# Kernel tuning notes

Measured on AMD Instinct MI355X. Metric: run time of the kernel, lower is better.

The kernel has to match this reference:

```python
import jax, jax.numpy as jnp
import numpy as np

B, N, D = 16, 2048, 128
SCALE = 1.0 / np.sqrt(D).astype(np.float32)


def setup_inputs() -> dict:
    key = jax.random.key(0)
    ks = jax.random.split(key, 9)
    Q = jax.random.normal(ks[0], (B, N, D), dtype=jnp.float32)
    K = jax.random.normal(ks[1], (B, N, D), dtype=jnp.float32)
    V = jax.random.normal(ks[2], (B, N, D), dtype=jnp.float32)
    bias_dis = 0.1 * jax.random.normal(ks[3], (N, N), dtype=jnp.float32)
    bias_dtw = 0.1 * jax.random.normal(ks[4], (N, N), dtype=jnp.float32)
    bias_pattern = 0.1 * jax.random.normal(ks[5], (N, N), dtype=jnp.float32)
    bias_poi = 0.1 * jax.random.normal(ks[6], (N, N), dtype=jnp.float32)
    # key/query padding masks: mostly True (valid) with some padding
    input_mask = jax.random.randint(ks[7], (B, N), 0, 10) > 0
    embeddings_mask = jax.random.randint(ks[8], (B, N), 0, 10) > 0
    # lower-triangular causal mask (diagonal kept so every row has a valid key)
    causal_mask = jnp.tril(jnp.ones((N, N), dtype=bool))
    return {"Q": Q, "K": K, "V": V, "bias_dis": bias_dis, "bias_dtw": bias_dtw,
            "bias_pattern": bias_pattern, "bias_poi": bias_poi,
            "input_mask": input_mask, "embeddings_mask": embeddings_mask,
            "causal_mask": causal_mask}


def reference(Q, K, V, bias_dis, bias_dtw, bias_pattern, bias_poi,
              input_mask, embeddings_mask, causal_mask):
    # masked_fill_(~mask, 0.0) on K, V with input_mask[:, :, None]
    km = input_mask[:, :, None]
    K = jnp.where(km, K, 0.0)
    V = jnp.where(km, V, 0.0)
    # masked_fill_(~mask, 0.0) on Q with embeddings_mask[:, :, None]
    Q = jnp.where(embeddings_mask[:, :, None], Q, 0.0)
    # scores [B, N, N] = Q K^T / sqrt(dim)
    scores = jnp.einsum('bnd,bmd->bnm', Q, K) * SCALE
    # causal masked_fill_(~causal_mask, -inf)
    scores = jnp.where(causal_mask[None, :, :], scores, -jnp.inf)
    # per-batch bias loop == broadcast add of summed [N, N] biases
    scores = scores + (bias_dis + bias_dtw + bias_pattern + bias_poi)[None, :, :]
    P = jax.nn.softmax(scores, axis=-1)
    # dropout p=0 (eval) -> identity
    return jnp.einsum('bnm,bmd->bnd', P, V)
```

## Files before the change

### kernel.cpp

```cpp
#include <hip/hip_runtime.h>
#include <math.h>

constexpr int Bc = 16;
constexpr int Nc = 2048;
constexpr int Dc = 128;
constexpr int NCHUNK = Nc / 64;
constexpr float SCALE_F = 0.08838834764831845f;

typedef __bf16 bf16x8 __attribute__((ext_vector_type(8)));
typedef __bf16 bf16x4 __attribute__((ext_vector_type(4)));
typedef float  f32x4  __attribute__((ext_vector_type(4)));

constexpr size_t KPACK_BYTES = (size_t)Bc * NCHUNK * 16 * 64 * 16;
constexpr size_t VPACK_BYTES = KPACK_BYTES;
constexpr size_t BIAS_BYTES  = (size_t)Nc * Nc * 4;
constexpr int CHUNK_ELEMS = 16 * 64 * 8;

__device__ __forceinline__ void gload_lds16(const __bf16* gsrc, __bf16* ldst) {
    __builtin_amdgcn_global_load_lds(
        (const __attribute__((address_space(1))) unsigned int*)gsrc,
        (__attribute__((address_space(3))) unsigned int*)ldst, 16, 0, 0);
}

__global__ __launch_bounds__(256) void bias_sum_kernel(
    const float* __restrict__ b0, const float* __restrict__ b1,
    const float* __restrict__ b2, const float* __restrict__ b3,
    float* __restrict__ bs)
{
    const int i = blockIdx.x * 256 + threadIdx.x;
    const float4 a = ((const float4*)b0)[i];
    const float4 c = ((const float4*)b1)[i];
    const float4 d = ((const float4*)b2)[i];
    const float4 e = ((const float4*)b3)[i];
    float4 r;
    r.x = a.x + c.x + d.x + e.x;
    r.y = a.y + c.y + d.y + e.y;
    r.z = a.z + c.z + d.z + e.z;
    r.w = a.w + c.w + d.w + e.w;
    ((float4*)bs)[i] = r;
}

__global__ __launch_bounds__(256) void pack_kv(
    const float* __restrict__ K, const float* __restrict__ V,
    const int* __restrict__ imask,
    __bf16* __restrict__ Kp, __bf16* __restrict__ Vp)
{
    __shared__ __align__(16) __bf16 Ks[64][136];
    __shared__ __align__(16) __bf16 Vs[64][136];
    const int tid = threadIdx.x;
    const int c = blockIdx.x, b = blockIdx.y;
    const int m0 = c * 64;
    const float* Kb = K + (size_t)b * Nc * Dc;
    const float* Vb = V + (size_t)b * Nc * Dc;
    const int* imb = imask + b * Nc;

    #pragma unroll
    for (int it = 0; it < 8; ++it) {
        const int idx = it * 256 + tid;
        const int row = idx >> 5;
        const int c4  = idx & 31;
        const int gm  = m0 + row;
        const float msk = imb[gm] ? 1.0f : 0.0f;
        const float4 kf = ((const float4*)(Kb + (size_t)gm * Dc))[c4];
        const float4 vf = ((const float4*)(Vb + (size_t)gm * Dc))[c4];
        bf16x4 kb, vb;
        kb[0] = (__bf16)(kf.x * msk); kb[1] = (__bf16)(kf.y * msk);
        kb[2] = (__bf16)(kf.z * msk); kb[3] = (__bf16)(kf.w * msk);
        vb[0] = (__bf16)(vf.x * msk); vb[1] = (__bf16)(vf.y * msk);
        vb[2] = (__bf16)(vf.z * msk); vb[3] = (__bf16)(vf.w * msk);
        *(bf16x4*)&Ks[row][c4 * 4] = kb;
        *(bf16x4*)&Vs[row][c4 * 4] = vb;
    }
    __syncthreads();

    const size_t chunk_base = (size_t)(b * NCHUNK + c) * CHUNK_ELEMS;
    #pragma unroll
    for (int i = 0; i < 4; ++i) {
        const int s = i * 256 + tid;
        const int f = s >> 6;
        const int l = s & 63;
        const int quad = (l >> 4) & 3;
        const int l15  = l & 15;
        {
            const int jt = f >> 2, kd = f & 3;
            const bf16x8 kv = *(const bf16x8*)&Ks[jt * 16 + l15][kd * 32 + quad * 8];
            *(bf16x8*)&Kp[chunk_base + (size_t)f * 512 + l * 8] = kv;
        }
        {
            const int kj = f >> 3, dt = f & 7;
            bf16x8 vv;
            #pragma unroll
            for (int j = 0; j < 8; ++j)
                vv[j] = Vs[kj * 32 + quad * 8 + j][dt * 16 + l15];
            *(bf16x8*)&Vp[chunk_base + (size_t)f * 512 + l * 8] = vv;
        }
    }
}

__global__ __launch_bounds__(256) void attn_packed(
    const float* __restrict__ Q,
    const __bf16* __restrict__ Kp, const __bf16* __restrict__ Vp,
    const float* __restrict__ p0, const float* __restrict__ p1,
    const float* __restrict__ p2, const float* __restrict__ p3,
    const int* __restrict__ emask, float* __restrict__ out, int nbias)
{
    __shared__ __align__(16) __bf16 Kl[16 * 512];
    __shared__ __align__(16) __bf16 Vl[16 * 512];
    __shared__ __align__(16) __bf16 Pl[4][16][72];

    const int tid  = threadIdx.x;
    const int w    = tid >> 6;
    const int lane = tid & 63;
    const int quad = lane >> 4;
    const int l15  = lane & 15;
    const int x = blockIdx.x, y = blockIdx.y;
    const int ti = (y < 8) ? x : (31 - x);
    const int b  = ((y & 7) << 1) | (y >> 3);
    const int q0  = ti * 64;
    const int q0w = q0 + w * 16;

    const float* Qb = Q + (size_t)b * Nc * Dc;

    bf16x8 qfrag[4];
    {
        const int row = q0w + l15;
        const float qs = emask[b * Nc + row] ? SCALE_F : 0.0f;
        const float4* qr = (const float4*)(Qb + (size_t)row * Dc);
        #pragma unroll
        for (int kd = 0; kd < 4; ++kd) {
            const float4 xx = qr[kd * 8 + quad * 2];
            const float4 yy = qr[kd * 8 + quad * 2 + 1];
            qfrag[kd][0] = (__bf16)(xx.x * qs); qfrag[kd][1] = (__bf16)(xx.y * qs);
            qfrag[kd][2] = (__bf16)(xx.z * qs); qfrag[kd][3] = (__bf16)(xx.w * qs);
            qfrag[kd][4] = (__bf16)(yy.x * qs); qfrag[kd][5] = (__bf16)(yy.y * qs);
            qfrag[kd][6] = (__bf16)(yy.z * qs); qfrag[kd][7] = (__bf16)(yy.w * qs);
        }
    }

    f32x4 oacc[8];
    #pragma unroll
    for (int dt = 0; dt < 8; ++dt) { oacc[dt][0]=0.f; oacc[dt][1]=0.f; oacc[dt][2]=0.f; oacc[dt][3]=0.f; }
    float mrun[4] = {-INFINITY, -INFINITY, -INFINITY, -INFINITY};
    float lrun[4] = {0.f, 0.f, 0.f, 0.f};

    for (int c = 0; c <= ti; ++c) {
        const int m0 = c * 64;
        __syncthreads();

        const __bf16* gK = Kp + (size_t)(b * NCHUNK + c) * CHUNK_ELEMS;
        const __bf16* gV = Vp + (size_t)(b * NCHUNK + c) * CHUNK_ELEMS;
        #pragma unroll
        for (int i = 0; i < 4; ++i) {
            const int seg = w * 4 + i;
            gload_lds16(gK + seg * 512 + lane * 8, Kl + seg * 512);
            gload_lds16(gV + seg * 512 + lane * 8, Vl + seg * 512);
        }

        float bsv[4][4];
        #pragma unroll
        for (int jt = 0; jt < 4; ++jt) {
            #pragma unroll
            for (int reg = 0; reg < 4; ++reg) {
                const int gr = q0w + quad * 4 + reg;
                const size_t boff = (size_t)gr * Nc + m0 + jt * 16 + l15;
                float v = p0[boff];
                if (nbias == 4) v += p1[boff] + p2[boff] + p3[boff];
                bsv[jt][reg] = v;
            }
        }
        __syncthreads();

        f32x4 sc[4];
        #pragma unroll
        for (int jt = 0; jt < 4; ++jt) { sc[jt][0]=0.f; sc[jt][1]=0.f; sc[jt][2]=0.f; sc[jt][3]=0.f; }
        #pragma unroll
        for (int jt = 0; jt < 4; ++jt) {
            #pragma unroll
            for (int kd = 0; kd < 4; ++kd) {
                const bf16x8 bfr = *(const bf16x8*)&Kl[(jt * 4 + kd) * 512 + lane * 8];
                sc[jt] = __builtin_amdgcn_mfma_f32_16x16x32_bf16(qfrag[kd], bfr, sc[jt], 0, 0, 0);
            }
        }

        if (c == ti) {
            #pragma unroll
            for (int jt = 0; jt < 4; ++jt)
                #pragma unroll
                for (int reg = 0; reg < 4; ++reg) {
                    const int gr = q0w + quad * 4 + reg;
                    const int gc = m0 + jt * 16 + l15;
                    const float s = sc[jt][reg] + bsv[jt][reg];
                    sc[jt][reg] = (gc > gr) ? -INFINITY : s;
                }
        } else {
            #pragma unroll
            for (int jt = 0; jt < 4; ++jt)
                #pragma unroll
                for (int reg = 0; reg < 4; ++reg)
                    sc[jt][reg] += bsv[jt][reg];
        }

        float mloc[4];
        #pragma unroll
        for (int reg = 0; reg < 4; ++reg)
            mloc[reg] = fmaxf(fmaxf(sc[0][reg], sc[1][reg]), fmaxf(sc[2][reg], sc[3][reg]));
        #pragma unroll
        for (int off = 1; off <= 8; off <<= 1)
            #pragma unroll
            for (int reg = 0; reg < 4; ++reg)
                mloc[reg] = fmaxf(mloc[reg], __shfl_xor(mloc[reg], off, 64));
        float lloc[4];
        #pragma unroll
        for (int reg = 0; reg < 4; ++reg) {
            const float mn = fmaxf(mrun[reg], mloc[reg]);
            const float alpha = __expf(mrun[reg] - mn);
            mrun[reg] = mn;
            lrun[reg] *= alpha;
            #pragma unroll
            for (int dt = 0; dt < 8; ++dt) oacc[dt][reg] *= alpha;
            float ls = 0.f;
            #pragma unroll
            for (int jt = 0; jt < 4; ++jt) {
                const float pv = __expf(sc[jt][reg] - mn);
                sc[jt][reg] = pv;
                ls += pv;
            }
            lloc[reg] = ls;
        }
        #pragma unroll
        for (int off = 1; off <= 8; off <<= 1)
            #pragma unroll
            for (int reg = 0; reg < 4; ++reg)
                lloc[reg] += __shfl_xor(lloc[reg], off, 64);
        #pragma unroll
        for (int reg = 0; reg < 4; ++reg) lrun[reg] += lloc[reg];

        #pragma unroll
        for (int jt = 0; jt < 4; ++jt)
            #pragma unroll
            for (int reg = 0; reg < 4; ++reg)
                Pl[w][quad * 4 + reg][jt * 16 + l15] = (__bf16)sc[jt][reg];

        #pragma unroll
        for (int kj = 0; kj < 2; ++kj) {
            const bf16x8 pa = *(const bf16x8*)&Pl[w][l15][kj * 32 + quad * 8];
            #pragma unroll
            for (int dt = 0; dt < 8; ++dt) {
                const bf16x8 vb = *(const bf16x8*)&Vl[(kj * 8 + dt) * 512 + lane * 8];
                oacc[dt] = __builtin_amdgcn_mfma_f32_16x16x32_bf16(pa, vb, oacc[dt], 0, 0, 0);
            }
        }
    }

    #pragma unroll
    for (int reg = 0; reg < 4; ++reg) {
        const float inv = 1.0f / lrun[reg];
        const int gr = q0w + quad * 4 + reg;
        float* orow = out + ((size_t)b * Nc + gr) * Dc;
        #pragma unroll
        for (int dt = 0; dt < 8; ++dt)
            orow[dt * 16 + l15] = oacc[dt][reg] * inv;
    }
}

__global__ __launch_bounds__(256) void attn_mfma_legacy(
    const float* __restrict__ Q, const float* __restrict__ K, const float* __restrict__ V,
    const float* __restrict__ p0, const float* __restrict__ p1,
    const float* __restrict__ p2, const float* __restrict__ p3,
    const int* __restrict__ imask, const int* __restrict__ emask,
    float* __restrict__ out, int nbias)
{
    __shared__ __align__(16) __bf16 Klds[64][136];
    __shared__ __align__(16) __bf16 Vt[128][72];
    __shared__ __align__(16) __bf16 Plds[4][16][72];
    const int tid  = threadIdx.x;
    const int w    = tid >> 6;
    const int lane = tid & 63;
    const int quad = lane >> 6 ? 0 : (lane >> 4);
    const int l15  = lane & 15;
    const int b = blockIdx.y;
    const int x = blockIdx.x, yy = blockIdx.y;
    const int ti = (yy < 8) ? x : (31 - x);
    const int q0 = ti * 64, q0w = q0 + w * 16;
    const float* Qb = Q + (size_t)b * Nc * Dc;
    const float* Kb = K + (size_t)b * Nc * Dc;
    const float* Vb = V + (size_t)b * Nc * Dc;
    const int* imb = imask + b * Nc;

    bf16x8 qfrag[4];
    {
        const int row = q0w + l15;
        const float qs = emask[b * Nc + row] ? SCALE_F : 0.0f;
        const float4* qr = (const float4*)(Qb + (size_t)row * Dc);
        #pragma unroll
        for (int kd = 0; kd < 4; ++kd) {
            const float4 xv = qr[kd * 8 + quad * 2];
            const float4 yv = qr[kd * 8 + quad * 2 + 1];
            qfrag[kd][0]=(__bf16)(xv.x*qs); qfrag[kd][1]=(__bf16)(xv.y*qs);
            qfrag[kd][2]=(__bf16)(xv.z*qs); qfrag[kd][3]=(__bf16)(xv.w*qs);
            qfrag[kd][4]=(__bf16)(yv.x*qs); qfrag[kd][5]=(__bf16)(yv.y*qs);
            qfrag[kd][6]=(__bf16)(yv.z*qs); qfrag[kd][7]=(__bf16)(yv.w*qs);
        }
    }
    f32x4 oacc[8];
    #pragma unroll
    for (int dt = 0; dt < 8; ++dt){oacc[dt][0]=0.f;oacc[dt][1]=0.f;oacc[dt][2]=0.f;oacc[dt][3]=0.f;}
    float mrun[4]={-INFINITY,-INFINITY,-INFINITY,-INFINITY}, lrun[4]={0.f,0.f,0.f,0.f};

    for (int m0 = 0; m0 <= q0; m0 += 64) {
        __syncthreads();
        #pragma unroll
        for (int it = 0; it < 8; ++it) {
            const int idx = it * 256 + tid;
            const int row = idx >> 5, c4 = idx & 31;
            const int gm = m0 + row;
            const float msk = imb[gm] ? 1.0f : 0.0f;
            const float4 kf = ((const float4*)(Kb + (size_t)gm * Dc))[c4];
            const float4 vf = ((const float4*)(Vb + (size_t)gm * Dc))[c4];
            bf16x4 kb;
            kb[0]=(__bf16)(kf.x*msk); kb[1]=(__bf16)(kf.y*msk);
            kb[2]=(__bf16)(kf.z*msk); kb[3]=(__bf16)(kf.w*msk);
            *(bf16x4*)&Klds[row][c4*4] = kb;
            Vt[c4*4+0][row]=(__bf16)(vf.x*msk); Vt[c4*4+1][row]=(__bf16)(vf.y*msk);
            Vt[c4*4+2][row]=(__bf16)(vf.z*msk); Vt[c4*4+3][row]=(__bf16)(vf.w*msk);
        }
        __syncthreads();
        f32x4 sc[4];
        #pragma unroll
        for (int jt = 0; jt < 4; ++jt){sc[jt][0]=0.f;sc[jt][1]=0.f;sc[jt][2]=0.f;sc[jt][3]=0.f;}
        #pragma unroll
        for (int jt = 0; jt < 4; ++jt)
            #pragma unroll
            for (int kd = 0; kd < 4; ++kd) {
                const bf16x8 bfr = *(const bf16x8*)&Klds[jt*16+l15][kd*32+quad*8];
                sc[jt] = __builtin_amdgcn_mfma_f32_16x16x32_bf16(qfrag[kd], bfr, sc[jt], 0, 0, 0);
            }
        #pragma unroll
        for (int jt = 0; jt < 4; ++jt)
            #pragma unroll
            for (int reg = 0; reg < 4; ++reg) {
                const int gr = q0w + quad*4 + reg;
                const int gc = m0 + jt*16 + l15;
                const size_t boff = (size_t)gr * Nc + gc;
                float bsx = p0[boff];
                if (nbias == 4) bsx += p1[boff] + p2[boff] + p3[boff];
                const float s = sc[jt][reg] + bsx;
                sc[jt][reg] = (gc > gr) ? -INFINITY : s;
            }
        float mloc[4];
        #pragma unroll
        for (int reg = 0; reg < 4; ++reg)
            mloc[reg] = fmaxf(fmaxf(sc[0][reg], sc[1][reg]), fmaxf(sc[2][reg], sc[3][reg]));
        #pragma unroll
        for (int off = 1; off <= 8; off <<= 1)
            #pragma unroll
            for (int reg = 0; reg < 4; ++reg)
                mloc[reg] = fmaxf(mloc[reg], __shfl_xor(mloc[reg], off, 64));
        float lloc[4];
        #pragma unroll
        for (int reg = 0; reg < 4; ++reg) {
            const float mn = fmaxf(mrun[reg], mloc[reg]);
            const float alpha = __expf(mrun[reg] - mn);
            mrun[reg] = mn; lrun[reg] *= alpha;
            #pragma unroll
            for (int dt = 0; dt < 8; ++dt) oacc[dt][reg] *= alpha;
            float ls = 0.f;
            #pragma unroll
            for (int jt = 0; jt < 4; ++jt) {
                const float pv = __expf(sc[jt][reg] - mn);
                sc[jt][reg] = pv; ls += pv;
            }
            lloc[reg] = ls;
        }
        #pragma unroll
        for (int off = 1; off <= 8; off <<= 1)
            #pragma unroll
            for (int reg = 0; reg < 4; ++reg)
                lloc[reg] += __shfl_xor(lloc[reg], off, 64);
        #pragma unroll
        for (int reg = 0; reg < 4; ++reg) lrun[reg] += lloc[reg];
        #pragma unroll
        for (int jt = 0; jt < 4; ++jt)
            #pragma unroll
            for (int reg = 0; reg < 4; ++reg)
                Plds[w][quad*4+reg][jt*16+l15] = (__bf16)sc[jt][reg];
        #pragma unroll
        for (int kj = 0; kj < 2; ++kj) {
            const bf16x8 pa = *(const bf16x8*)&Plds[w][l15][kj*32+quad*8];
            #pragma unroll
            for (int dt = 0; dt < 8; ++dt) {
                const bf16x8 vb = *(const bf16x8*)&Vt[dt*16+l15][kj*32+quad*8];
                oacc[dt] = __builtin_amdgcn_mfma_f32_16x16x32_bf16(pa, vb, oacc[dt], 0, 0, 0);
            }
        }
    }
    #pragma unroll
    for (int reg = 0; reg < 4; ++reg) {
        const float inv = 1.0f / lrun[reg];
        const int gr = q0w + quad*4 + reg;
        float* orow = out + ((size_t)b * Nc + gr) * Dc;
        #pragma unroll
        for (int dt = 0; dt < 8; ++dt)
            orow[dt*16+l15] = oacc[dt][reg] * inv;
    }
}

extern "C" void kernel_launch(void* const* d_in, const int* in_sizes, int n_in,
                              void* d_out, int out_size, void* d_ws, size_t ws_size,
                              hipStream_t stream) {
    const float* Q  = (const float*)d_in[0];
    const float* K  = (const float*)d_in[1];
    const float* V  = (const float*)d_in[2];
    const float* b0 = (const float*)d_in[3];
    const float* b1 = (const float*)d_in[4];
    const float* b2 = (const float*)d_in[5];
    const float* b3 = (const float*)d_in[6];
    const int* im   = (const int*)d_in[7];
    const int* em   = (const int*)d_in[8];
    float* out      = (float*)d_out;

    const dim3 grid(NCHUNK, Bc);
    const bool havePacks = ws_size >= KPACK_BYTES + VPACK_BYTES;
    const bool haveBias  = ws_size >= KPACK_BYTES + VPACK_BYTES + BIAS_BYTES;

    if (havePacks) {
        __bf16* Kp = (__bf16*)d_ws;
        __bf16* Vp = (__bf16*)((char*)d_ws + KPACK_BYTES);
        pack_kv<<<grid, 256, 0, stream>>>(K, V, im, Kp, Vp);
        if (haveBias) {
            float* bs = (float*)((char*)d_ws + KPACK_BYTES + VPACK_BYTES);
            bias_sum_kernel<<<(Nc * Nc / 4) / 256, 256, 0, stream>>>(b0, b1, b2, b3, bs);
            attn_packed<<<grid, 256, 0, stream>>>(Q, Kp, Vp, bs, bs, bs, bs, em, out, 1);
        } else {
            attn_packed<<<grid, 256, 0, stream>>>(Q, Kp, Vp, b0, b1, b2, b3, em, out, 4);
        }
    } else if (ws_size >= BIAS_BYTES) {
        float* bs = (float*)d_ws;
        bias_sum_kernel<<<(Nc * Nc / 4) / 256, 256, 0, stream>>>(b0, b1, b2, b3, bs);
        attn_mfma_legacy<<<grid, 256, 0, stream>>>(Q, K, V, bs, bs, bs, bs, im, em, out, 1);
    } else {
        attn_mfma_legacy<<<grid, 256, 0, stream>>>(Q, K, V, b0, b1, b2, b3, im, em, out, 4);
    }
}
```

Measured before the change: 237.1 us.

## Fuse prep kernels, pair causal query tiles per block, double-buffer K/V loads

Merges the K/V packing and bias-summing kernels into one launch to save a launch and let the two jobs overlap. The attention kernel now gives each block two query tiles (p and 31-p) of the same batch so every block does equal causal work, using a 16x16 grid instead of 32x16. K/V chunks are double-buffered in LDS and the next chunk's bias is prefetched into registers while the current chunk is computed, hiding load latency. The cost is half as many blocks (256), which may lower occupancy and parallelism on a large GPU, plus more LDS and register use.

```diff
diff --git a/kernel.cpp b/kernel.cpp
--- a/kernel.cpp
+++ b/kernel.cpp
@@ -22,33 +22,35 @@
         (__attribute__((address_space(3))) unsigned int*)ldst, 16, 0, 0);
 }
 
-__global__ __launch_bounds__(256) void bias_sum_kernel(
+__global__ __launch_bounds__(256) void prep_fused(
+    const float* __restrict__ K, const float* __restrict__ V,
+    const int* __restrict__ imask,
     const float* __restrict__ b0, const float* __restrict__ b1,
     const float* __restrict__ b2, const float* __restrict__ b3,
-    float* __restrict__ bs)
-{
-    const int i = blockIdx.x * 256 + threadIdx.x;
-    const float4 a = ((const float4*)b0)[i];
-    const float4 c = ((const float4*)b1)[i];
-    const float4 d = ((const float4*)b2)[i];
-    const float4 e = ((const float4*)b3)[i];
-    float4 r;
-    r.x = a.x + c.x + d.x + e.x;
-    r.y = a.y + c.y + d.y + e.y;
-    r.z = a.z + c.z + d.z + e.z;
-    r.w = a.w + c.w + d.w + e.w;
-    ((float4*)bs)[i] = r;
-}
-
-__global__ __launch_bounds__(256) void pack_kv(
-    const float* __restrict__ K, const float* __restrict__ V,
-    const int* __restrict__ imask,
-    __bf16* __restrict__ Kp, __bf16* __restrict__ Vp)
+    __bf16* __restrict__ Kp, __bf16* __restrict__ Vp, float* __restrict__ bs)
 {
     __shared__ __align__(16) __bf16 Ks[64][136];
     __shared__ __align__(16) __bf16 Vs[64][136];
+    const int bid = blockIdx.x;
     const int tid = threadIdx.x;
-    const int c = blockIdx.x, b = blockIdx.y;
+
+    if (bid >= 512) {
+        const int i = (bid - 512) * 256 + tid;
+        const float4 a = ((const float4*)b0)[i];
+        const float4 c = ((const float4*)b1)[i];
+        const float4 d = ((const float4*)b2)[i];
+        const float4 e = ((const float4*)b3)[i];
+        float4 r;
+        r.x = a.x + c.x + d.x + e.x;
+        r.y = a.y + c.y + d.y + e.y;
+        r.z = a.z + c.z + d.z + e.z;
+        r.w = a.w + c.w + d.w + e.w;
+        ((float4*)bs)[i] = r;
+        return;
+    }
+
+    const int c = bid & 31;
+    const int b = bid >> 5;
     const int m0 = c * 64;
     const float* Kb = K + (size_t)b * Nc * Dc;
     const float* Vb = V + (size_t)b * Nc * Dc;
@@ -97,15 +99,14 @@
     }
 }
 
-__global__ __launch_bounds__(256) void attn_packed(
+__global__ __launch_bounds__(256) void attn_paired(
     const float* __restrict__ Q,
     const __bf16* __restrict__ Kp, const __bf16* __restrict__ Vp,
-    const float* __restrict__ p0, const float* __restrict__ p1,
-    const float* __restrict__ p2, const float* __restrict__ p3,
-    const int* __restrict__ emask, float* __restrict__ out, int nbias)
+    const float* __restrict__ bias, const int* __restrict__ emask,
+    float* __restrict__ out)
 {
-    __shared__ __align__(16) __bf16 Kl[16 * 512];
-    __shared__ __align__(16) __bf16 Vl[16 * 512];
+    __shared__ __align__(16) __bf16 Kl[2][16 * 512];
+    __shared__ __align__(16) __bf16 Vl[2][16 * 512];
     __shared__ __align__(16) __bf16 Pl[4][16][72];
 
     const int tid  = threadIdx.x;
@@ -113,153 +114,179 @@
     const int lane = tid & 63;
     const int quad = lane >> 4;
     const int l15  = lane & 15;
-    const int x = blockIdx.x, y = blockIdx.y;
-    const int ti = (y < 8) ? x : (31 - x);
-    const int b  = ((y & 7) << 1) | (y >> 3);
-    const int q0  = ti * 64;
-    const int q0w = q0 + w * 16;
-
-    const float* Qb = Q + (size_t)b * Nc * Dc;
-
-    bf16x8 qfrag[4];
-    {
-        const int row = q0w + l15;
-        const float qs = emask[b * Nc + row] ? SCALE_F : 0.0f;
-        const float4* qr = (const float4*)(Qb + (size_t)row * Dc);
-        #pragma unroll
-        for (int kd = 0; kd < 4; ++kd) {
-            const float4 xx = qr[kd * 8 + quad * 2];
-            const float4 yy = qr[kd * 8 + quad * 2 + 1];
-            qfrag[kd][0] = (__bf16)(xx.x * qs); qfrag[kd][1] = (__bf16)(xx.y * qs);
-            qfrag[kd][2] = (__bf16)(xx.z * qs); qfrag[kd][3] = (__bf16)(xx.w * qs);
-            qfrag[kd][4] = (__bf16)(yy.x * qs); qfrag[kd][5] = (__bf16)(yy.y * qs);
-            qfrag[kd][6] = (__bf16)(yy.z * qs); qfrag[kd][7] = (__bf16)(yy.w * qs);
-        }
-    }
-
-    f32x4 oacc[8];
-    #pragma unroll
-    for (int dt = 0; dt < 8; ++dt) { oacc[dt][0]=0.f; oacc[dt][1]=0.f; oacc[dt][2]=0.f; oacc[dt][3]=0.f; }
-    float mrun[4] = {-INFINITY, -INFINITY, -INFINITY, -INFINITY};
-    float lrun[4] = {0.f, 0.f, 0.f, 0.f};
-
-    for (int c = 0; c <= ti; ++c) {
-        const int m0 = c * 64;
-        __syncthreads();
-
-        const __bf16* gK = Kp + (size_t)(b * NCHUNK + c) * CHUNK_ELEMS;
-        const __bf16* gV = Vp + (size_t)(b * NCHUNK + c) * CHUNK_ELEMS;
+    const int b = blockIdx.x;
+    const int p = blockIdx.y;
+
+    const float*  Qb  = Q + (size_t)b * Nc * Dc;
+    const int*    emb = emask + b * Nc;
+    const __bf16* Kpb = Kp + (size_t)b * NCHUNK * CHUNK_ELEMS;
+    const __bf16* Vpb = Vp + (size_t)b * NCHUNK * CHUNK_ELEMS;
+
+    for (int t = 0; t < 2; ++t) {
+        const int ti  = t ? (31 - p) : p;
+        const int q0w = ti * 64 + w * 16;
+        const int nch = ti + 1;
+
+        bf16x8 qfrag[4];
+        {
+            const int row = q0w + l15;
+            const float qs = emb[row] ? SCALE_F : 0.0f;
+            const float4* qr = (const float4*)(Qb + (size_t)row * Dc);
+            #pragma unroll
+            for (int kd = 0; kd < 4; ++kd) {
+                const float4 xx = qr[kd * 8 + quad * 2];
+                const float4 yy = qr[kd * 8 + quad * 2 + 1];
+                qfrag[kd][0] = (__bf16)(xx.x * qs); qfrag[kd][1] = (__bf16)(xx.y * qs);
+                qfrag[kd][2] = (__bf16)(xx.z * qs); qfrag[kd][3] = (__bf16)(xx.w * qs);
+                qfrag[kd][4] = (__bf16)(yy.x * qs); qfrag[kd][5] = (__bf16)(yy.y * qs);
+                qfrag[kd][6] = (__bf16)(yy.z * qs); qfrag[kd][7] = (__bf16)(yy.w * qs);
+            }
+        }
+
+        f32x4 oacc[8];
+        #pragma unroll
+        for (int dt = 0; dt < 8; ++dt) { oacc[dt][0]=0.f; oacc[dt][1]=0.f; oacc[dt][2]=0.f; oacc[dt][3]=0.f; }
+        float mrun[4] = {-INFINITY, -INFINITY, -INFINITY, -INFINITY};
+        float lrun[4] = {0.f, 0.f, 0.f, 0.f};
+
         #pragma unroll
         for (int i = 0; i < 4; ++i) {
             const int seg = w * 4 + i;
-            gload_lds16(gK + seg * 512 + lane * 8, Kl + seg * 512);
-            gload_lds16(gV + seg * 512 + lane * 8, Vl + seg * 512);
-        }
-
-        float bsv[4][4];
-        #pragma unroll
-        for (int jt = 0; jt < 4; ++jt) {
+            gload_lds16(Kpb + seg * 512 + lane * 8, &Kl[0][seg * 512]);
+            gload_lds16(Vpb + seg * 512 + lane * 8, &Vl[0][seg * 512]);
+        }
+        float bcur[4][4];
+        #pragma unroll
+        for (int jt = 0; jt < 4; ++jt)
+            #pragma unroll
+            for (int reg = 0; reg < 4; ++reg)
+                bcur[jt][reg] = bias[(size_t)(q0w + quad * 4 + reg) * Nc + jt * 16 + l15];
+        __syncthreads();
+
+        for (int c = 0; c < nch; ++c) {
+            const int cb = c & 1;
+            const bool more = (c + 1) < nch;
+
+            if (more) {
+                const size_t off = (size_t)(c + 1) * CHUNK_ELEMS;
+                #pragma unroll
+                for (int i = 0; i < 4; ++i) {
+                    const int seg = w * 4 + i;
+                    gload_lds16(Kpb + off + seg * 512 + lane * 8, &Kl[cb ^ 1][seg * 512]);
+                    gload_lds16(Vpb + off + seg * 512 + lane * 8, &Vl[cb ^ 1][seg * 512]);
+                }
+            }
+            float bnext[4][4];
+            if (more) {
+                const int m1 = (c + 1) * 64;
+                #pragma unroll
+                for (int jt = 0; jt < 4; ++jt)
+                    #pragma unroll
+                    for (int reg = 0; reg < 4; ++reg)
+                        bnext[jt][reg] = bias[(size_t)(q0w + quad * 4 + reg) * Nc + m1 + jt * 16 + l15];
+            }
+
+            f32x4 sc[4];
+            #pragma unroll
+            for (int jt = 0; jt < 4; ++jt) { sc[jt][0]=0.f; sc[jt][1]=0.f; sc[jt][2]=0.f; sc[jt][3]=0.f; }
+            #pragma unroll
+            for (int jt = 0; jt < 4; ++jt)
+                #pragma unroll
+                for (int kd = 0; kd < 4; ++kd) {
+                    const bf16x8 bfr = *(const bf16x8*)&Kl[cb][(jt * 4 + kd) * 512 + lane * 8];
+                    sc[jt] = __builtin_amdgcn_mfma_f32_16x16x32_bf16(qfrag[kd], bfr, sc[jt], 0, 0, 0);
+                }
+
+            if (c == ti) {
+                const int m0 = c * 64;
+                #pragma unroll
+                for (int jt = 0; jt < 4; ++jt)
+                    #pragma unroll
+                    for (int reg = 0; reg < 4; ++reg) {
+                        const int gr = q0w + quad * 4 + reg;
+                        const int gc = m0 + jt * 16 + l15;
+                        const float s = sc[jt][reg] + bcur[jt][reg];
+                        sc[jt][reg] = (gc > gr) ? -INFINITY : s;
+                    }
+            } else {
+                #pragma unroll
+                for (int jt = 0; jt < 4; ++jt)
+                    #pragma unroll
+                    for (int reg = 0; reg < 4; ++reg)
+                        sc[jt][reg] += bcur[jt][reg];
+            }
+
+            float mloc[4];
+            #pragma unroll
+            for (int reg = 0; reg < 4; ++reg)
+                mloc[reg] = fmaxf(fmaxf(sc[0][reg], sc[1][reg]), fmaxf(sc[2][reg], sc[3][reg]));
+            #pragma unroll
+            for (int off = 1; off <= 8; off <<= 1)
+                #pragma unroll
+                for (int reg = 0; reg < 4; ++reg)
+                    mloc[reg] = fmaxf(mloc[reg], __shfl_xor(mloc[reg], off, 64));
+            float lloc[4];
             #pragma unroll
             for (int reg = 0; reg < 4; ++reg) {
-                const int gr = q0w + quad * 4 + reg;
-                const size_t boff = (size_t)gr * Nc + m0 + jt * 16 + l15;
-                float v = p0[boff];
-                if (nbias == 4) v += p1[boff] + p2[boff] + p3[boff];
-                bsv[jt][reg] = v;
-            }
-        }
-        __syncthreads();
-
-        f32x4 sc[4];
-        #pragma unroll
-        for (int jt = 0; jt < 4; ++jt) { sc[jt][0]=0.f; sc[jt][1]=0.f; sc[jt][2]=0.f; sc[jt][3]=0.f; }
-        #pragma unroll
-        for (int jt = 0; jt < 4; ++jt) {
-            #pragma unroll
-            for (int kd = 0; kd < 4; ++kd) {
-                const bf16x8 bfr = *(const bf16x8*)&Kl[(jt * 4 + kd) * 512 + lane * 8];
-                sc[jt] = __builtin_amdgcn_mfma_f32_16x16x32_bf16(qfrag[kd], bfr, sc[jt], 0, 0, 0);
-            }
-        }
-
-        if (c == ti) {
+                const float mn = fmaxf(mrun[reg], mloc[reg]);
+                const float alpha = __expf(mrun[reg] - mn);
+                mrun[reg] = mn;
+                lrun[reg] *= alpha;
+                #pragma unroll
+                for (int dt = 0; dt < 8; ++dt) oacc[dt][reg] *= alpha;
+                float ls = 0.f;
+                #pragma unroll
+                for (int jt = 0; jt < 4; ++jt) {
+                    const float pv = __expf(sc[jt][reg] - mn);
+                    sc[jt][reg] = pv;
+                    ls += pv;
+                }
+                lloc[reg] = ls;
+            }
+            #pragma unroll
+            for (int off = 1; off <= 8; off <<= 1)
+                #pragma unroll
+                for (int reg = 0; reg < 4; ++reg)
+                    lloc[reg] += __shfl_xor(lloc[reg], off, 64);
+            #pragma unroll
+            for (int reg = 0; reg < 4; ++reg) lrun[reg] += lloc[reg];
+
             #pragma unroll
             for (int jt = 0; jt < 4; ++jt)
                 #pragma unroll
-                for (int reg = 0; reg < 4; ++reg) {
-                    const int gr = q0w + quad * 4 + reg;
-                    const int gc = m0 + jt * 16 + l15;
-                    const float s = sc[jt][reg] + bsv[jt][reg];
-                    sc[jt][reg] = (gc > gr) ? -INFINITY : s;
+                for (int reg = 0; reg < 4; ++reg)
+                    Pl[w][quad * 4 + reg][jt * 16 + l15] = (__bf16)sc[jt][reg];
+
+            #pragma unroll
+            for (int kj = 0; kj < 2; ++kj) {
+                const bf16x8 pa = *(const bf16x8*)&Pl[w][l15][kj * 32 + quad * 8];
+                #pragma unroll
+                for (int dt = 0; dt < 8; ++dt) {
+                    const bf16x8 vb = *(const bf16x8*)&Vl[cb][(kj * 8 + dt) * 512 + lane * 8];
+                    oacc[dt] = __builtin_amdgcn_mfma_f32_16x16x32_bf16(pa, vb, oacc[dt], 0, 0, 0);
                 }
-        } else {
-            #pragma unroll
-            for (int jt = 0; jt < 4; ++jt)
-                #pragma unroll
-                for (int reg = 0; reg < 4; ++reg)
-                    sc[jt][reg] += bsv[jt][reg];
-        }
-
-        float mloc[4];
-        #pragma unroll
-        for (int reg = 0; reg < 4; ++reg)
-            mloc[reg] = fmaxf(fmaxf(sc[0][reg], sc[1][reg]), fmaxf(sc[2][reg], sc[3][reg]));
-        #pragma unroll
-        for (int off = 1; off <= 8; off <<= 1)
-            #pragma unroll
-            for (int reg = 0; reg < 4; ++reg)
-                mloc[reg] = fmaxf(mloc[reg], __shfl_xor(mloc[reg], off, 64));
-        float lloc[4];
+            }
+
+            __syncthreads();
+
+            if (more) {
+                #pragma unroll
+                for (int jt = 0; jt < 4; ++jt)
+                    #pragma unroll
+                    for (int reg = 0; reg < 4; ++reg)
+                        bcur[jt][reg] = bnext[jt][reg];
+            }
+        }
+
         #pragma unroll
         for (int reg = 0; reg < 4; ++reg) {
-            const float mn = fmaxf(mrun[reg], mloc[reg]);
-            const float alpha = __expf(mrun[reg] - mn);
-            mrun[reg] = mn;
-            lrun[reg] *= alpha;
-            #pragma unroll
-            for (int dt = 0; dt < 8; ++dt) oacc[dt][reg] *= alpha;
-            float ls = 0.f;
-            #pragma unroll
-            for (int jt = 0; jt < 4; ++jt) {
-                const float pv = __expf(sc[jt][reg] - mn);
-                sc[jt][reg] = pv;
-                ls += pv;
-            }
-            lloc[reg] = ls;
-        }
-        #pragma unroll
-        for (int off = 1; off <= 8; off <<= 1)
-            #pragma unroll
-            for (int reg = 0; reg < 4; ++reg)
-                lloc[reg] += __shfl_xor(lloc[reg], off, 64);
-        #pragma unroll
-        for (int reg = 0; reg < 4; ++reg) lrun[reg] += lloc[reg];
-
-        #pragma unroll
-        for (int jt = 0; jt < 4; ++jt)
-            #pragma unroll
-            for (int reg = 0; reg < 4; ++reg)
-                Pl[w][quad * 4 + reg][jt * 16 + l15] = (__bf16)sc[jt][reg];
-
-        #pragma unroll
-        for (int kj = 0; kj < 2; ++kj) {
-            const bf16x8 pa = *(const bf16x8*)&Pl[w][l15][kj * 32 + quad * 8];
-            #pragma unroll
-            for (int dt = 0; dt < 8; ++dt) {
-                const bf16x8 vb = *(const bf16x8*)&Vl[(kj * 8 + dt) * 512 + lane * 8];
-                oacc[dt] = __builtin_amdgcn_mfma_f32_16x16x32_bf16(pa, vb, oacc[dt], 0, 0, 0);
-            }
-        }
-    }
-
-    #pragma unroll
-    for (int reg = 0; reg < 4; ++reg) {
-        const float inv = 1.0f / lrun[reg];
-        const int gr = q0w + quad * 4 + reg;
-        float* orow = out + ((size_t)b * Nc + gr) * Dc;
-        #pragma unroll
-        for (int dt = 0; dt < 8; ++dt)
-            orow[dt * 16 + l15] = oacc[dt][reg] * inv;
+            const float inv = 1.0f / lrun[reg];
+            const int gr = q0w + quad * 4 + reg;
+            float* orow = out + ((size_t)b * Nc + gr) * Dc;
+            #pragma unroll
+            for (int dt = 0; dt < 8; ++dt)
+                orow[dt * 16 + l15] = oacc[dt][reg] * inv;
+        }
     }
 }
 
@@ -268,7 +295,7 @@
     const float* __restrict__ p0, const float* __restrict__ p1,
     const float* __restrict__ p2, const float* __restrict__ p3,
     const int* __restrict__ imask, const int* __restrict__ emask,
-    float* __restrict__ out, int nbias)
+    float* __restrict__ out)
 {
     __shared__ __align__(16) __bf16 Klds[64][136];
     __shared__ __align__(16) __bf16 Vt[128][72];
@@ -276,7 +303,7 @@
     const int tid  = threadIdx.x;
     const int w    = tid >> 6;
     const int lane = tid & 63;
-    const int quad = lane >> 6 ? 0 : (lane >> 4);
+    const int quad = lane >> 4;
     const int l15  = lane & 15;
     const int b = blockIdx.y;
     const int x = blockIdx.x, yy = blockIdx.y;
@@ -342,8 +369,7 @@
                 const int gr = q0w + quad*4 + reg;
                 const int gc = m0 + jt*16 + l15;
                 const size_t boff = (size_t)gr * Nc + gc;
-                float bsx = p0[boff];
-                if (nbias == 4) bsx += p1[boff] + p2[boff] + p3[boff];
+                const float bsx = p0[boff] + p1[boff] + p2[boff] + p3[boff];
                 const float s = sc[jt][reg] + bsx;
                 sc[jt][reg] = (gc > gr) ? -INFINITY : s;
             }
@@ -419,26 +445,15 @@
     const int* em   = (const int*)d_in[8];
     float* out      = (float*)d_out;
 
-    const dim3 grid(NCHUNK, Bc);
-    const bool havePacks = ws_size >= KPACK_BYTES + VPACK_BYTES;
-    const bool haveBias  = ws_size >= KPACK_BYTES + VPACK_BYTES + BIAS_BYTES;
-
-    if (havePacks) {
+    if (ws_size >= KPACK_BYTES + VPACK_BYTES + BIAS_BYTES) {
         __bf16* Kp = (__bf16*)d_ws;
         __bf16* Vp = (__bf16*)((char*)d_ws + KPACK_BYTES);
-        pack_kv<<<grid, 256, 0, stream>>>(K, V, im, Kp, Vp);
-        if (haveBias) {
-            float* bs = (float*)((char*)d_ws + KPACK_BYTES + VPACK_BYTES);
-            bias_sum_kernel<<<(Nc * Nc / 4) / 256, 256, 0, stream>>>(b0, b1, b2, b3, bs);
-            attn_packed<<<grid, 256, 0, stream>>>(Q, Kp, Vp, bs, bs, bs, bs, em, out, 1);
-        } else {
-            attn_packed<<<grid, 256, 0, stream>>>(Q, Kp, Vp, b0, b1, b2, b3, em, out, 4);
-        }
-    } else if (ws_size >= BIAS_BYTES) {
-        float* bs = (float*)d_ws;
-        bias_sum_kernel<<<(Nc * Nc / 4) / 256, 256, 0, stream>>>(b0, b1, b2, b3, bs);
-        attn_mfma_legacy<<<grid, 256, 0, stream>>>(Q, K, V, bs, bs, bs, bs, im, em, out, 1);
+        float*  bs = (float*)((char*)d_ws + KPACK_BYTES + VPACK_BYTES);
+        prep_fused<<<512 + (Nc * Nc / 4) / 256, 256, 0, stream>>>(
+            K, V, im, b0, b1, b2, b3, Kp, Vp, bs);
+        attn_paired<<<dim3(Bc, 16), 256, 0, stream>>>(Q, Kp, Vp, bs, em, out);
     } else {
-        attn_mfma_legacy<<<grid, 256, 0, stream>>>(Q, K, V, b0, b1, b2, b3, im, em, out, 4);
+        attn_mfma_legacy<<<dim3(NCHUNK, Bc), 256, 0, stream>>>(
+            Q, K, V, b0, b1, b2, b3, im, em, out);
     }
 }
```

Measured after the change: 237.1 us. About the same (-0.0%).
